# Optimization experiments

Measured on AMD Instinct MI355X. Metric: run time of the kernel, lower is better.

## Reference

```python
import jax, jax.numpy as jnp
import numpy as np

L_MAX = 3
C = 512  # channels per degree


def _triples(l_max):
    ts = []
    for l1 in range(l_max + 1):
        for l2 in range(l1, l_max + 1):
            for L in range(l2 - l1, min(l_max, l1 + l2) + 1):
                ts.append((l1, l2, L))
    return ts


def setup_inputs() -> dict:
    key = jax.random.key(0)
    keys = jax.random.split(key, 4 + len(_triples(L_MAX)))
    inp = {}
    ki = 0
    for l in range(L_MAX + 1):
        inp[f"x{l}"] = jax.random.normal(keys[ki], (C, 2 * l + 1), dtype=jnp.float32)
        ki += 1
    for (l1, l2, L) in _triples(L_MAX):
        # cg[L, l2, l1] has shape [2L+1, 2l2+1, 2l1+1]
        inp[f"cg_{L}_{l2}_{l1}"] = 0.1 * jax.random.normal(
            keys[ki], (2 * L + 1, 2 * l2 + 1, 2 * l1 + 1), dtype=jnp.float32)
        ki += 1
    return inp


def reference(x0, x1, x2, x3,
              cg_0_0_0, cg_1_1_0, cg_2_2_0, cg_3_3_0,
              cg_0_1_1, cg_1_1_1, cg_2_1_1, cg_1_2_1, cg_2_2_1, cg_3_2_1,
              cg_2_3_1, cg_3_3_1,
              cg_0_2_2, cg_1_2_2, cg_2_2_2, cg_3_2_2, cg_1_3_2, cg_2_3_2,
              cg_3_3_2,
              cg_0_3_3, cg_1_3_3, cg_2_3_3, cg_3_3_3):
    xs = [x0, x1, x2, x3]
    cg_list = [cg_0_0_0, cg_1_1_0, cg_2_2_0, cg_3_3_0,
               cg_0_1_1, cg_1_1_1, cg_2_1_1, cg_1_2_1, cg_2_2_1, cg_3_2_1,
               cg_2_3_1, cg_3_3_1,
               cg_0_2_2, cg_1_2_2, cg_2_2_2, cg_3_2_2, cg_1_3_2, cg_2_3_2,
               cg_3_3_2,
               cg_0_3_3, cg_1_3_3, cg_2_3_3, cg_3_3_3]
    cg = dict(zip(_triples(L_MAX), cg_list))
    out = {L: [] for L in range(L_MAX + 1)}
    for (l1, l2, L) in _triples(L_MAX):
        # product: [i, j, 2L+1]
        p = jnp.einsum('Mnm,im,jn->ijM', cg[(l1, l2, L)], xs[l1], xs[l2])
        out[L].append(p.reshape(-1, 2 * L + 1))
    return tuple(jnp.concatenate(out[L], axis=0) for L in range(L_MAX + 1))
```

## Files before the change

### kernel.cpp

```cpp
#include <hip/hip_runtime.h>


#define C2 (512 * 512)

struct Ptrs {
    const float* x[4];
    const float* cg[23];
};

#define TRIPLE_LIST(F) \
    F(0, 0, 0, 0, 0, 0) \
    F(1, 0, 1, 1, 4, 1) \
    F(2, 0, 2, 2, 22, 10) \
    F(3, 0, 3, 3, 57, 35) \
    F(4, 1, 1, 0, 1, 84) \
    F(5, 1, 1, 1, 7, 87) \
    F(6, 1, 1, 2, 27, 96) \
    F(7, 1, 2, 1, 10, 111) \
    F(8, 1, 2, 2, 32, 126) \
    F(9, 1, 2, 3, 64, 151) \
    F(10, 1, 3, 2, 37, 186) \
    F(11, 1, 3, 3, 71, 221) \
    F(12, 2, 2, 0, 2, 270) \
    F(13, 2, 2, 1, 13, 275) \
    F(14, 2, 2, 2, 42, 290) \
    F(15, 2, 2, 3, 78, 315) \
    F(16, 2, 3, 1, 16, 350) \
    F(17, 2, 3, 2, 47, 371) \
    F(18, 2, 3, 3, 85, 406) \
    F(19, 3, 3, 0, 3, 455) \
    F(20, 3, 3, 1, 19, 462) \
    F(21, 3, 3, 2, 52, 483) \
    F(22, 3, 3, 3, 92, 518)

#define XBASE(L2) ((L2) == 0 ? 0 : ((L2) == 1 ? 1 : ((L2) == 2 ? 4 : 9)))

__global__ __launch_bounds__(256) void cg_tp_kernel(Ptrs p, float* __restrict__ out) {
    __shared__ float smem[16 * 256];
    __shared__ float ysh[567];

    const int tid = threadIdx.x;
    const int b = blockIdx.x;
    const int i = b >> 1;
    const int j0 = (b & 1) << 8;

    {
        float* xT = smem;
        const float* xp0 = p.x[0] + j0;
        xT[0 * 256 + tid] = xp0[tid];

        const float* xp1 = p.x[1] + j0 * 3;
        #pragma unroll
        for (int r = 0; r < 3; ++r) {
            int idx = tid + r * 256;
            xT[(1 + idx % 3) * 256 + idx / 3] = xp1[idx];
        }
        const float* xp2 = p.x[2] + j0 * 5;
        #pragma unroll
        for (int r = 0; r < 5; ++r) {
            int idx = tid + r * 256;
            xT[(4 + idx % 5) * 256 + idx / 5] = xp2[idx];
        }
        const float* xp3 = p.x[3] + j0 * 7;
        #pragma unroll
        for (int r = 0; r < 7; ++r) {
            int idx = tid + r * 256;
            xT[(9 + idx % 7) * 256 + idx / 7] = xp3[idx];
        }
    }

    for (int e = tid; e < 567; e += 256) {
#define YC(T, L1, L2, LL, OB, YO)                                              \
        if (e >= (YO) && e < (YO) + (2 * L2 + 1) * (2 * LL + 1)) {             \
            const int local = e - (YO);                                        \
            const int n = local / (2 * LL + 1);                                \
            const int M = local % (2 * LL + 1);                                \
            const float* cg = p.cg[T] + (M * (2 * L2 + 1) + n) * (2 * L1 + 1); \
            const float* xi = p.x[L1] + i * (2 * L1 + 1);                      \
            float s = 0.f;                                                     \
            _Pragma("unroll")                                                  \
            for (int m = 0; m < 2 * L1 + 1; ++m) s = fmaf(cg[m], xi[m], s);    \
            ysh[e] = s;                                                        \
        }
        TRIPLE_LIST(YC)
#undef YC
    }

    __syncthreads();

    float xj[16];
    #pragma unroll
    for (int k = 0; k < 16; ++k) xj[k] = smem[k * 256 + tid];

    __syncthreads();

#define TC(T, L1, L2, LL, OB, YO)                                              \
    {                                                                          \
        constexpr int NW = 2 * LL + 1;                                         \
        float acc[NW] = {};                                                    \
        const float* y = ysh + (YO);                                           \
        _Pragma("unroll")                                                      \
        for (int n = 0; n < 2 * L2 + 1; ++n) {                                 \
            const float xv = xj[XBASE(L2) + n];                                \
            _Pragma("unroll")                                                  \
            for (int M = 0; M < NW; ++M)                                       \
                acc[M] = fmaf(y[n * NW + M], xv, acc[M]);                      \
        }                                                                      \
        float* stg = smem + ((T) & 1) * (7 * 256);                             \
        _Pragma("unroll")                                                      \
        for (int M = 0; M < NW; ++M) stg[tid * NW + M] = acc[M];               \
        __syncthreads();                                                       \
        const float4* s4 = (const float4*)stg;                                 \
        float4* dst = (float4*)(out + (size_t)(OB) * C2 + (size_t)b * (256 * NW)); \
        for (int k = tid; k < 64 * NW; k += 256) dst[k] = s4[k];               \
    }
    TRIPLE_LIST(TC)
#undef TC
}

extern "C" void kernel_launch(void* const* d_in, const int* in_sizes, int n_in,
                              void* d_out, int out_size, void* d_ws, size_t ws_size,
                              hipStream_t stream) {
    Ptrs p;
    for (int l = 0; l < 4; ++l) p.x[l] = (const float*)d_in[l];
    for (int t = 0; t < 23; ++t) p.cg[t] = (const float*)d_in[4 + t];
    cg_tp_kernel<<<dim3(1024), dim3(256), 0, stream>>>(p, (float*)d_out);
}
```

Measured before the change: 171.3 us.

## Split work into one block per triple and row with templated specialization

```diff
diff --git a/kernel.cpp b/kernel.cpp
--- a/kernel.cpp
+++ b/kernel.cpp
@@ -9,113 +9,96 @@
 };
 
 #define TRIPLE_LIST(F) \
-    F(0, 0, 0, 0, 0, 0) \
-    F(1, 0, 1, 1, 4, 1) \
-    F(2, 0, 2, 2, 22, 10) \
-    F(3, 0, 3, 3, 57, 35) \
-    F(4, 1, 1, 0, 1, 84) \
-    F(5, 1, 1, 1, 7, 87) \
-    F(6, 1, 1, 2, 27, 96) \
-    F(7, 1, 2, 1, 10, 111) \
-    F(8, 1, 2, 2, 32, 126) \
-    F(9, 1, 2, 3, 64, 151) \
-    F(10, 1, 3, 2, 37, 186) \
-    F(11, 1, 3, 3, 71, 221) \
-    F(12, 2, 2, 0, 2, 270) \
-    F(13, 2, 2, 1, 13, 275) \
-    F(14, 2, 2, 2, 42, 290) \
-    F(15, 2, 2, 3, 78, 315) \
-    F(16, 2, 3, 1, 16, 350) \
-    F(17, 2, 3, 2, 47, 371) \
-    F(18, 2, 3, 3, 85, 406) \
-    F(19, 3, 3, 0, 3, 455) \
-    F(20, 3, 3, 1, 19, 462) \
-    F(21, 3, 3, 2, 52, 483) \
-    F(22, 3, 3, 3, 92, 518)
+    F(0, 0, 0, 0, 0) \
+    F(1, 0, 1, 1, 4) \
+    F(2, 0, 2, 2, 22) \
+    F(3, 0, 3, 3, 57) \
+    F(4, 1, 1, 0, 1) \
+    F(5, 1, 1, 1, 7) \
+    F(6, 1, 1, 2, 27) \
+    F(7, 1, 2, 1, 10) \
+    F(8, 1, 2, 2, 32) \
+    F(9, 1, 2, 3, 64) \
+    F(10, 1, 3, 2, 37) \
+    F(11, 1, 3, 3, 71) \
+    F(12, 2, 2, 0, 2) \
+    F(13, 2, 2, 1, 13) \
+    F(14, 2, 2, 2, 42) \
+    F(15, 2, 2, 3, 78) \
+    F(16, 2, 3, 1, 16) \
+    F(17, 2, 3, 2, 47) \
+    F(18, 2, 3, 3, 85) \
+    F(19, 3, 3, 0, 3) \
+    F(20, 3, 3, 1, 19) \
+    F(21, 3, 3, 2, 52) \
+    F(22, 3, 3, 3, 92)
 
-#define XBASE(L2) ((L2) == 0 ? 0 : ((L2) == 1 ? 1 : ((L2) == 2 ? 4 : 9)))
+template <int T, int L1, int L2, int LL, int OB>
+__device__ __forceinline__ void triple_block(
+        const Ptrs& p, float* __restrict__ out, int i, int tid,
+        float* __restrict__ xT, float* __restrict__ ys, float* __restrict__ stg) {
+    constexpr int NI = 2 * L1 + 1;
+    constexpr int NJ = 2 * L2 + 1;
+    constexpr int NW = 2 * LL + 1;
+
+    {
+        const float4* src4 = (const float4*)p.x[L2];
+        float4* dst4 = (float4*)xT;
+        #pragma unroll
+        for (int k = tid; k < 128 * NJ; k += 256) dst4[k] = src4[k];
+    }
+
+    if (tid < NJ * NW) {
+        const int n = tid / NW;
+        const int M = tid % NW;
+        const float* cg = p.cg[T] + (M * NJ + n) * NI;
+        const float* xi = p.x[L1] + i * NI;
+        float s = 0.f;
+        #pragma unroll
+        for (int m = 0; m < NI; ++m) s = fmaf(cg[m], xi[m], s);
+        ys[tid] = s;
+    }
+    __syncthreads();
+
+    float xj0[NJ], xj1[NJ];
+    #pragma unroll
+    for (int n = 0; n < NJ; ++n) {
+        xj0[n] = xT[tid * NJ + n];
+        xj1[n] = xT[(tid + 256) * NJ + n];
+    }
+    #pragma unroll
+    for (int M = 0; M < NW; ++M) {
+        float a0 = 0.f, a1 = 0.f;
+        #pragma unroll
+        for (int n = 0; n < NJ; ++n) {
+            const float yv = ys[n * NW + M];
+            a0 = fmaf(xj0[n], yv, a0);
+            a1 = fmaf(xj1[n], yv, a1);
+        }
+        stg[tid * NW + M] = a0;
+        stg[(tid + 256) * NW + M] = a1;
+    }
+    __syncthreads();
+
+    const float4* s4 = (const float4*)stg;
+    float4* dst = (float4*)(out + (size_t)OB * C2 + (size_t)i * (512 * NW));
+    #pragma unroll
+    for (int k = tid; k < 128 * NW; k += 256) dst[k] = s4[k];
+}
 
 __global__ __launch_bounds__(256) void cg_tp_kernel(Ptrs p, float* __restrict__ out) {
-    __shared__ float smem[16 * 256];
-    __shared__ float ysh[567];
-
+    __shared__ float xT[512 * 7];
+    __shared__ float ys[7 * 7];
+    __shared__ float stg[512 * 7];
     const int tid = threadIdx.x;
-    const int b = blockIdx.x;
-    const int i = b >> 1;
-    const int j0 = (b & 1) << 8;
-
-    {
-        float* xT = smem;
-        const float* xp0 = p.x[0] + j0;
-        xT[0 * 256 + tid] = xp0[tid];
-
-        const float* xp1 = p.x[1] + j0 * 3;
-        #pragma unroll
-        for (int r = 0; r < 3; ++r) {
-            int idx = tid + r * 256;
-            xT[(1 + idx % 3) * 256 + idx / 3] = xp1[idx];
-        }
-        const float* xp2 = p.x[2] + j0 * 5;
-        #pragma unroll
-        for (int r = 0; r < 5; ++r) {
-            int idx = tid + r * 256;
-            xT[(4 + idx % 5) * 256 + idx / 5] = xp2[idx];
-        }
-        const float* xp3 = p.x[3] + j0 * 7;
-        #pragma unroll
-        for (int r = 0; r < 7; ++r) {
-            int idx = tid + r * 256;
-            xT[(9 + idx % 7) * 256 + idx / 7] = xp3[idx];
-        }
+    const int t = blockIdx.x >> 9;
+    const int i = blockIdx.x & 511;
+    switch (t) {
+#define TCASE(T, L1, L2, LL, OB) \
+        case T: triple_block<T, L1, L2, LL, OB>(p, out, i, tid, xT, ys, stg); break;
+        TRIPLE_LIST(TCASE)
+#undef TCASE
     }
-
-    for (int e = tid; e < 567; e += 256) {
-#define YC(T, L1, L2, LL, OB, YO)                                              \
-        if (e >= (YO) && e < (YO) + (2 * L2 + 1) * (2 * LL + 1)) {             \
-            const int local = e - (YO);                                        \
-            const int n = local / (2 * LL + 1);                                \
-            const int M = local % (2 * LL + 1);                                \
-            const float* cg = p.cg[T] + (M * (2 * L2 + 1) + n) * (2 * L1 + 1); \
-            const float* xi = p.x[L1] + i * (2 * L1 + 1);                      \
-            float s = 0.f;                                                     \
-            _Pragma("unroll")                                                  \
-            for (int m = 0; m < 2 * L1 + 1; ++m) s = fmaf(cg[m], xi[m], s);    \
-            ysh[e] = s;                                                        \
-        }
-        TRIPLE_LIST(YC)
-#undef YC
-    }
-
-    __syncthreads();
-
-    float xj[16];
-    #pragma unroll
-    for (int k = 0; k < 16; ++k) xj[k] = smem[k * 256 + tid];
-
-    __syncthreads();
-
-#define TC(T, L1, L2, LL, OB, YO)                                              \
-    {                                                                          \
-        constexpr int NW = 2 * LL + 1;                                         \
-        float acc[NW] = {};                                                    \
-        const float* y = ysh + (YO);                                           \
-        _Pragma("unroll")                                                      \
-        for (int n = 0; n < 2 * L2 + 1; ++n) {                                 \
-            const float xv = xj[XBASE(L2) + n];                                \
-            _Pragma("unroll")                                                  \
-            for (int M = 0; M < NW; ++M)                                       \
-                acc[M] = fmaf(y[n * NW + M], xv, acc[M]);                      \
-        }                                                                      \
-        float* stg = smem + ((T) & 1) * (7 * 256);                             \
-        _Pragma("unroll")                                                      \
-        for (int M = 0; M < NW; ++M) stg[tid * NW + M] = acc[M];               \
-        __syncthreads();                                                       \
-        const float4* s4 = (const float4*)stg;                                 \
-        float4* dst = (float4*)(out + (size_t)(OB) * C2 + (size_t)b * (256 * NW)); \
-        for (int k = tid; k < 64 * NW; k += 256) dst[k] = s4[k];               \
-    }
-    TRIPLE_LIST(TC)
-#undef TC
 }
 
 extern "C" void kernel_launch(void* const* d_in, const int* in_sizes, int n_in,
@@ -124,5 +107,5 @@
     Ptrs p;
     for (int l = 0; l < 4; ++l) p.x[l] = (const float*)d_in[l];
     for (int t = 0; t < 23; ++t) p.cg[t] = (const float*)d_in[4 + t];
-    cg_tp_kernel<<<dim3(1024), dim3(256), 0, stream>>>(p, (float*)d_out);
+    cg_tp_kernel<<<dim3(23 * 512), dim3(256), 0, stream>>>(p, (float*)d_out);
 }
```

New measurement: 178.2 us. +4.0%, slower.
